# Kernel tuning notes

Hardware: AMD Instinct MI355X
Metric: run time of the kernel (lower is better)

## Reference

```python
import jax, jax.numpy as jnp
import numpy as np

B, N, D = 32, 540, 512
H = 8
DH = D // H
MAX_LEN = 540
POS_CLIP = MAX_LEN - 1


def setup_inputs() -> dict:
    key = jax.random.key(0)
    ks = jax.random.split(key, 12)
    s = 0.02
    inp = {
        "query": jax.random.normal(ks[0], (B, N, D), dtype=jnp.float32),
        "Wq": jax.random.normal(ks[1], (D, D), dtype=jnp.float32) * s,
        "bq": jnp.zeros((D,), jnp.float32),
        "Wk": jax.random.normal(ks[2], (D, D), dtype=jnp.float32) * s,
        "bk": jnp.zeros((D,), jnp.float32),
        "Wv": jax.random.normal(ks[3], (D, D), dtype=jnp.float32) * s,
        "bv": jnp.zeros((D,), jnp.float32),
        "Wh": jax.random.normal(ks[4], (D, D), dtype=jnp.float32) * s,
        "bh": jnp.zeros((D,), jnp.float32),
        "pos_k": jax.random.uniform(ks[5], (2 * POS_CLIP + 1, DH), dtype=jnp.float32, minval=-0.05, maxval=0.05),
        "gamma": jnp.ones((D,), jnp.float32),
        "beta": jnp.zeros((D,), jnp.float32),
        "valid_len": jax.random.randint(ks[6], (B,), 1, N + 1, dtype=jnp.int32),
    }
    return inp


def _split_heads(x):
    # [B, N, D] -> [H*B, N, DH], head-major on axis 0 (matches tf.concat(tf.split(x,H,-1),0))
    return x.reshape(B, N, H, DH).transpose(2, 0, 1, 3).reshape(H * B, N, DH)


def reference(query, Wq, bq, Wk, bk, Wv, bv, Wh, bh, pos_k, gamma, beta, valid_len):
    q = _split_heads(query @ Wq + bq)  # [HB, N, DH]
    k = _split_heads(query @ Wk + bk)
    v = _split_heads(query @ Wv + bv)

    QK = jnp.einsum("xqd,xkd->xqk", q, k)  # [HB, N, N]

    # relative position bias (Shaw et al. 2018)
    rel = jnp.arange(N)[None, :] - jnp.arange(N)[:, None]
    rel = jnp.clip(rel, -POS_CLIP, POS_CLIP) + POS_CLIP
    pos_enc_k = pos_k[rel]  # [N, N, DH]
    QR = jnp.einsum("xqd,qkd->xqk", q, pos_enc_k)

    attn = (QK + QR) / jnp.sqrt(jnp.float32(DH))

    # key-side sequence mask, broadcast over heads and query rows
    key_mask = jnp.arange(N)[None, :] < valid_len[:, None]  # [B, N]
    key_mask = jnp.tile(key_mask[:, None, :], (H, N, 1))  # [HB, N, N]
    attn = jnp.where(key_mask, attn, jnp.float32(-1e12))
    attn = jax.nn.softmax(attn, axis=-1)

    out = jnp.einsum("xqk,xkd->xqd", attn, v)  # [HB, N, DH]
    out = out.reshape(H, B, N, DH).transpose(1, 2, 0, 3).reshape(B, N, D)
    out = out @ Wh + bh
    out = out + query

    # layer norm over last axis
    mean = jnp.mean(out, axis=-1, keepdims=True)
    var = jnp.mean(jnp.square(out - mean), axis=-1, keepdims=True)
    normalized = (out - mean) * jax.lax.rsqrt(var + 1e-7)
    return gamma * normalized + beta
```

## Files before the change

### kernel.cpp

```cpp
#include <hip/hip_runtime.h>
#include <hip/hip_bf16.h>

typedef __hip_bfloat16 bf16;

#define NB 32
#define NSEQ 540
#define ND 512
#define NH 8
#define NDH 64
#define NHB 256
#define NM 17280
#define NPOS 1079
#define VTP 544

typedef __bf16 v8bf __attribute__((ext_vector_type(8)));
typedef float f32x4 __attribute__((ext_vector_type(4)));

union U8 {
  uint4 u;
  unsigned short s[8];
  v8bf v;
};

union U2 {
  uint2 u;
  unsigned short s[4];
};

__device__ __forceinline__ unsigned short f2b(float x) {
  union { float f; unsigned u; } c;
  c.f = x;
  const unsigned r = c.u + 0x7fffu + ((c.u >> 16) & 1u);
  return (unsigned short)(r >> 16);
}

__device__ __forceinline__ float b2f16(unsigned short s) {
  return __uint_as_float(((unsigned)s) << 16);
}

__device__ __forceinline__ void bar_lds() {
  asm volatile("s_waitcnt lgkmcnt(0)\n\ts_barrier" ::: "memory");
}

__device__ __forceinline__ int xcd_swz(int p, int total) {
  const int g = p >> 5, r = p & 31;
  return ((g << 5) + 32 <= total) ? ((g << 5) + ((r & 7) << 2) + (r >> 3)) : p;
}

__device__ __forceinline__ void gl_lds16(const unsigned short* g,
                                         unsigned short* l) {
  __builtin_amdgcn_global_load_lds(
      (const __attribute__((address_space(1))) unsigned int*)g,
      (__attribute__((address_space(3))) unsigned int*)l, 16, 0, 0);
}

__device__ __forceinline__ void cvt16(const float* __restrict__ p,
                                      unsigned short* __restrict__ dst) {
  unsigned short s[16];
#pragma unroll
  for (int i = 0; i < 4; i++) {
    const float4 v = *(const float4*)(p + i * 4);
    s[i * 4 + 0] = f2b(v.x);
    s[i * 4 + 1] = f2b(v.y);
    s[i * 4 + 2] = f2b(v.z);
    s[i * 4 + 3] = f2b(v.w);
  }
  *(uint4*)dst = *(uint4*)s;
  *(uint4*)(dst + 8) = *(uint4*)(s + 8);
}

__global__ __launch_bounds__(256) void prep(const float* __restrict__ x,
                                            unsigned short* __restrict__ xb,
                                            const float* __restrict__ pos,
                                            unsigned short* __restrict__ posb) {
  const int blk = blockIdx.x;
  if (blk < 4320) {
    const int i = blk * 256 + threadIdx.x;
    const float4 a = *(const float4*)(x + (size_t)i * 8);
    const float4 b = *(const float4*)(x + (size_t)i * 8 + 4);
    unsigned short s[8];
    s[0] = f2b(a.x); s[1] = f2b(a.y); s[2] = f2b(a.z); s[3] = f2b(a.w);
    s[4] = f2b(b.x); s[5] = f2b(b.y); s[6] = f2b(b.z); s[7] = f2b(b.w);
    *(uint4*)(xb + (size_t)i * 8) = *(uint4*)s;
  } else {
    const int i = (blk - 4320) * 256 + threadIdx.x;
    if (i < NPOS * NDH) posb[i] = f2b(pos[i]);
  }
}

__global__ __launch_bounds__(256) void wcvt(
    const float* __restrict__ Wq, const float* __restrict__ Wk,
    const float* __restrict__ Wv, const float* __restrict__ Wh,
    unsigned short* __restrict__ Wt) {
  __shared__ unsigned short T[64][72];
  const int tid = threadIdx.x;
  const int sel = blockIdx.z;
  const float* W = (sel == 0) ? Wq : (sel == 1) ? Wk : (sel == 2) ? Wv : Wh;
  unsigned short* out = Wt + (size_t)sel * ND * ND;
  const int k0 = blockIdx.x * 64, n0 = blockIdx.y * 64;
  const int r = tid >> 2, g = tid & 3;
  cvt16(W + (size_t)(k0 + r) * ND + n0 + g * 16, &T[r][g * 16]);
  __syncthreads();
  unsigned short s[16];
#pragma unroll
  for (int j = 0; j < 16; j++) s[j] = T[g * 16 + j][r];
  unsigned short* dst = out + (size_t)(n0 + r) * ND + k0 + g * 16;
  *(uint4*)dst = *(uint4*)s;
  *(uint4*)(dst + 8) = *(uint4*)(s + 8);
}

#define GEMM_CORE_B16(APTR)                                                       \
  {                                                                               \
    const int lrow = lane >> 2;                                                   \
    const int lc8 = (lane & 3) * 8;                                               \
    const int arow = 32 * w + lrow;                   \
    const unsigned short* ga = APTR + (size_t)(m0 + arow) * ND + lc8;             \
    const unsigned short* gb = Bt + (size_t)(n0 + arow) * ND + lc8;               \
    gl_lds16(ga, &As[0][(2 * w) * 512]);                                          \
    gl_lds16(ga + 16 * ND, &As[0][(2 * w) * 512 + 512]);                          \
    gl_lds16(gb, &Bs[0][(2 * w) * 512]);                                          \
    gl_lds16(gb + 16 * ND, &Bs[0][(2 * w) * 512 + 512]);                          \
    __syncthreads();                                                              \
    for (int t = 0; t < 16; t++) {                                                \
      const int cur = t & 1;                                                      \
      if (t < 15) {                                                               \
        const int k1 = (t + 1) * 32;                                              \
        gl_lds16(ga + k1, &As[cur ^ 1][(2 * w) * 512]);                           \
        gl_lds16(ga + k1 + 16 * ND, &As[cur ^ 1][(2 * w) * 512 + 512]);           \
        gl_lds16(gb + k1, &Bs[cur ^ 1][(2 * w) * 512]);                           \
        gl_lds16(gb + k1 + 16 * ND, &Bs[cur ^ 1][(2 * w) * 512 + 512]);           \
      }                                                                           \
      U8 af[4], bfr[4];                                                           \
      _Pragma("unroll")                                                           \
      for (int mi = 0; mi < 4; mi++)                                              \
        af[mi].u = *(const uint4*)&As[cur][(wr * 64 + mi * 16 + l15) * 32 +       \
                                           quad * 8];                             \
      _Pragma("unroll")                                                           \
      for (int ni = 0; ni < 4; ni++)                                              \
        bfr[ni].u = *(const uint4*)&Bs[cur][(wc * 64 + ni * 16 + l15) * 32 +      \
                                            quad * 8];                            \
      _Pragma("unroll")                                                           \
      for (int mi = 0; mi < 4; mi++)                                              \
        _Pragma("unroll")                                                         \
        for (int ni = 0; ni < 4; ni++)                                            \
          acc[mi][ni] = __builtin_amdgcn_mfma_f32_16x16x32_bf16(                  \
              af[mi].v, bfr[ni].v, acc[mi][ni], 0, 0, 0);                         \
      __syncthreads();                                                            \
    }                                                                             \
  }

__global__ __launch_bounds__(256, 3) void qkv_mfma(
    const unsigned short* __restrict__ Xb, const unsigned short* __restrict__ Wt,
    const float* __restrict__ bq, const float* __restrict__ bk,
    const float* __restrict__ bv,
    bf16* __restrict__ qh, bf16* __restrict__ kh, bf16* __restrict__ vt) {
  __shared__ unsigned short As[2][4096];
  __shared__ unsigned short Bs[2][4096];
  const int tid = threadIdx.x;
  const int phys = blockIdx.x + (blockIdx.y << 2) + 540 * blockIdx.z;
  const int W = xcd_swz(phys, 1620);
  const int sel = W / 540;
  const int rem = W - sel * 540;
  const int m0 = (rem >> 2) * 128, n0 = (rem & 3) * 128;
  const unsigned short* Bt = Wt + (size_t)sel * ND * ND;
  const float* bias = (sel == 0) ? bq : (sel == 1) ? bk : bv;
  const int lane = tid & 63, w = tid >> 6;
  const int wr = w & 1, wc = w >> 1;
  const int l15 = lane & 15, quad = lane >> 4;

  f32x4 acc[4][4];
#pragma unroll
  for (int mi = 0; mi < 4; mi++)
#pragma unroll
    for (int ni = 0; ni < 4; ni++) acc[mi][ni] = (f32x4){0.f, 0.f, 0.f, 0.f};

  GEMM_CORE_B16(Xb)

  if (sel != 2) {
    unsigned short* o = (unsigned short*)((sel == 0) ? qh : kh);
#pragma unroll
    for (int mi = 0; mi < 4; mi++) {
      const int m = m0 + wr * 64 + mi * 16 + quad * 4;
      const int bidx = m / NSEQ;
      const int seq0 = m - bidx * NSEQ;
#pragma unroll
      for (int ni = 0; ni < 4; ni++) {
        const int n = n0 + wc * 64 + ni * 16 + l15;
        const int h = n >> 6, dh = n & 63;
        const float bsv = bias[n];
        const size_t base = (((size_t)(h * NB + bidx)) * NSEQ + seq0) * NDH + dh;
#pragma unroll
        for (int i = 0; i < 4; i++)
          o[base + (size_t)i * NDH] = f2b(acc[mi][ni][i] + bsv);
      }
    }
  } else {
    unsigned short* o = (unsigned short*)vt;
#pragma unroll
    for (int mi = 0; mi < 4; mi++) {
      const int m = m0 + wr * 64 + mi * 16 + quad * 4;
      const int bidx = m / NSEQ;
      const int seq0 = m - bidx * NSEQ;
#pragma unroll
      for (int ni = 0; ni < 4; ni++) {
        const int n = n0 + wc * 64 + ni * 16 + l15;
        const int h = n >> 6, dh = n & 63;
        const float bsv = bias[n];
        unsigned short pk[4];
#pragma unroll
        for (int i = 0; i < 4; i++) pk[i] = f2b(acc[mi][ni][i] + bsv);
        *(uint2*)(o + (((size_t)(h * NB + bidx)) * NDH + dh) * VTP + seq0) =
            *(uint2*)pk;
      }
    }
  }
}

__global__ __launch_bounds__(256, 3) void out_mfma(
    const unsigned short* __restrict__ ctxb, const unsigned short* __restrict__ Wht,
    const float* __restrict__ bh, const float* __restrict__ query,
    float* __restrict__ tmp) {
  __shared__ unsigned short As[2][4096];
  __shared__ unsigned short Bs[2][4096];
  const int tid = threadIdx.x;
  const unsigned short* Bt = Wht;
  const int phys = blockIdx.x + (blockIdx.y << 2);
  const int W = xcd_swz(phys, 540);
  const int m0 = (W >> 2) * 128, n0 = (W & 3) * 128;
  const int lane = tid & 63, w = tid >> 6;
  const int wr = w & 1, wc = w >> 1;
  const int l15 = lane & 15, quad = lane >> 4;

  f32x4 acc[4][4];
#pragma unroll
  for (int mi = 0; mi < 4; mi++)
#pragma unroll
    for (int ni = 0; ni < 4; ni++) acc[mi][ni] = (f32x4){0.f, 0.f, 0.f, 0.f};

  GEMM_CORE_B16(ctxb)

#pragma unroll
  for (int mi = 0; mi < 4; mi++) {
    const int m = m0 + wr * 64 + mi * 16 + quad * 4;
#pragma unroll
    for (int ni = 0; ni < 4; ni++) {
      const int n = n0 + wc * 64 + ni * 16 + l15;
      const float bsv = bh[n];
#pragma unroll
      for (int i = 0; i < 4; i++) {
        const size_t off = (size_t)(m + i) * ND + n;
        tmp[off] = acc[mi][ni][i] + bsv + query[off];
      }
    }
  }
}

#define PW 584

__global__ __launch_bounds__(256, 6) void attn(
    const bf16* __restrict__ qh, const bf16* __restrict__ kh,
    const bf16* __restrict__ vt, const unsigned short* __restrict__ posb,
    const int* __restrict__ vlen, bf16* __restrict__ ctx) {
  __shared__ unsigned short P[16][PW];
  __shared__ float Tt[16][84];
  __shared__ float red4[16][4];
  __shared__ float sinv[16];

  const int tid = threadIdx.x;
  const int lane = tid & 63;
  const int w = tid >> 6;
  const int l15 = lane & 15;
  const int quad = lane >> 4;
  const int qb = blockIdx.x;
  const int x = blockIdx.y;
  const int b = x & 31, h = x >> 5;
  const int q0 = qb * 16;
  const int valid = vlen[b];
  const int NT = (valid + 63) >> 6;
  const int NC = (valid + 31) >> 5;
  const bf16* qbase = qh + (size_t)x * NSEQ * NDH;
  const unsigned short* kbase = (const unsigned short*)(kh + (size_t)x * NSEQ * NDH);
  const unsigned short* vbase = (const unsigned short*)(vt + (size_t)x * NDH * VTP);

  U8 aq0, aq1;
  {
    const int q = q0 + l15;
    if (q < NSEQ) {
      aq0.u = *(const uint4*)(qbase + (size_t)q * NDH + quad * 8);
      aq1.u = *(const uint4*)(qbase + (size_t)q * NDH + 32 + quad * 8);
    } else {
      aq0.u = make_uint4(0, 0, 0, 0);
      aq1.u = make_uint4(0, 0, 0, 0);
    }
  }

  U8 ck0, ck1, cp0, cp1, ce0, ce1;
  {
    const int key = w * 16 + l15;
    ck0.u = *(const uint4*)(kbase + (size_t)key * NDH + quad * 8);
    ck1.u = *(const uint4*)(kbase + (size_t)key * NDH + 32 + quad * 8);
    const long pr = (long)(524 - q0 + w * 16 + l15);
    cp0.u = *(const uint4*)(posb + pr * NDH + quad * 8);
    cp1.u = *(const uint4*)(posb + pr * NDH + 32 + quad * 8);
    if (w == 0) {
      const long pr2 = (long)(524 - q0 + 64 + l15);
      ce0.u = *(const uint4*)(posb + pr2 * NDH + quad * 8);
      ce1.u = *(const uint4*)(posb + pr2 * NDH + 32 + quad * 8);
    }
  }

  float pmax1 = -1e30f;

  for (int kt = 0; kt < NT; kt++) {
    U8 nk0, nk1, np0, np1, ne0, ne1;
    if (kt < NT - 1) {
      const int k1 = kt * 64 + 64;
      const int key = k1 + w * 16 + l15;
      nk0.u = *(const uint4*)(kbase + (size_t)key * NDH + quad * 8);
      nk1.u = *(const uint4*)(kbase + (size_t)key * NDH + 32 + quad * 8);
      const long pr = (long)(k1 - q0 + 524 + w * 16 + l15);
      np0.u = *(const uint4*)(posb + pr * NDH + quad * 8);
      np1.u = *(const uint4*)(posb + pr * NDH + 32 + quad * 8);
      if (w == 0) {
        const long pr2 = (long)(k1 - q0 + 524 + 64 + l15);
        ne0.u = *(const uint4*)(posb + pr2 * NDH + quad * 8);
        ne1.u = *(const uint4*)(posb + pr2 * NDH + 32 + quad * 8);
      }
    }

    f32x4 accqk = {0.f, 0.f, 0.f, 0.f};
    accqk = __builtin_amdgcn_mfma_f32_16x16x32_bf16(ck0.v, aq0.v, accqk, 0, 0, 0);
    accqk = __builtin_amdgcn_mfma_f32_16x16x32_bf16(ck1.v, aq1.v, accqk, 0, 0, 0);
    f32x4 accT = {0.f, 0.f, 0.f, 0.f};
    accT = __builtin_amdgcn_mfma_f32_16x16x32_bf16(cp0.v, aq0.v, accT, 0, 0, 0);
    accT = __builtin_amdgcn_mfma_f32_16x16x32_bf16(cp1.v, aq1.v, accT, 0, 0, 0);
    f32x4 accT2 = {0.f, 0.f, 0.f, 0.f};
    if (w == 0) {
      accT2 = __builtin_amdgcn_mfma_f32_16x16x32_bf16(ce0.v, aq0.v, accT2, 0, 0, 0);
      accT2 = __builtin_amdgcn_mfma_f32_16x16x32_bf16(ce1.v, aq1.v, accT2, 0, 0, 0);
    }

    bar_lds();
    *(f32x4*)&Tt[l15][w * 16 + quad * 4] = accT;
    if (w == 0) *(f32x4*)&Tt[l15][64 + quad * 4] = accT2;
    bar_lds();
    {
      const int k0 = kt * 64;
      const int cb = w * 16 + quad * 4;
      const int jb = cb + 15 - l15;
      U2 pk;
      float pm = -1e30f;
#pragma unroll
      for (int i = 0; i < 4; i++) {
        const float v = (accqk[i] + Tt[l15][jb + i]) * 0.125f;
        pk.s[i] = f2b(v);
        const bool cm = (k0 + cb + i) < valid;
        pm = fmaxf(pm, cm ? v : -1e30f);
      }
      *(uint2*)&P[l15][k0 + cb] = pk.u;
      pmax1 = fmaxf(pmax1, pm);
    }
    ck0 = nk0; ck1 = nk1; cp0 = np0; cp1 = np1;
    if (w == 0) { ce0 = ne0; ce1 = ne1; }
  }

  pmax1 = fmaxf(pmax1, __shfl_xor(pmax1, 16, 64));
  pmax1 = fmaxf(pmax1, __shfl_xor(pmax1, 32, 64));
  if (quad == 0) red4[l15][w] = pmax1;

  const int dh = w * 16 + l15;
  const unsigned short* vrow = vbase + (size_t)dh * VTP;
  U8 cv;
  cv.u = *(const uint4*)(vrow + quad * 8);

  bar_lds();

  {
    const int r = tid >> 4, c = tid & 15;
    const float4 rm = *(const float4*)red4[r];
    const float rowmax = fmaxf(fmaxf(rm.x, rm.y), fmaxf(rm.z, rm.w));
    const int nv = (valid + 7) >> 3;
    float sl = 0.f;
    for (int ch = c; ch < nv; ch += 16) {
      const uint4 u = *(const uint4*)&P[r][ch * 8];
      unsigned ue[4];
#pragma unroll
      for (int jj = 0; jj < 4; jj++) {
        const unsigned uu = ((const unsigned*)&u)[jj];
        const float lo = __uint_as_float(uu << 16);
        const float hi = __uint_as_float(uu & 0xffff0000u);
        float el = __expf(lo - rowmax);
        float eh = __expf(hi - rowmax);
        const int cb = ch * 8 + jj * 2;
        el = (cb < valid) ? el : 0.f;
        eh = (cb + 1 < valid) ? eh : 0.f;
        sl += el + eh;
        ue[jj] = (unsigned)f2b(el) | ((unsigned)f2b(eh) << 16);
      }
      *(uint4*)&P[r][ch * 8] = *(const uint4*)ue;
    }
    for (int ch = c; ch < 72; ch += 16) {
      if (ch >= nv) *(uint4*)&P[r][ch * 8] = make_uint4(0, 0, 0, 0);
    }
#pragma unroll
    for (int m = 1; m < 16; m <<= 1) sl += __shfl_xor(sl, m, 16);
    if (c == 0) sinv[r] = 1.f / sl;
  }
  bar_lds();

  f32x4 acco = {0.f, 0.f, 0.f, 0.f};
  for (int ci = 0; ci < NC; ci++) {
    U8 nv_;
    if (ci + 1 < NC) nv_.u = *(const uint4*)(vrow + (ci + 1) * 32 + quad * 8);
    U8 ap;
    ap.u = *(const uint4*)&P[l15][ci * 32 + quad * 8];
    acco = __builtin_amdgcn_mfma_f32_16x16x32_bf16(ap.v, cv.v, acco, 0, 0, 0);
    cv = nv_;
  }
  unsigned short* ob = (unsigned short*)ctx;
#pragma unroll
  for (int i = 0; i < 4; i++) {
    const int q = q0 + quad * 4 + i;
    if (q < NSEQ) {
      ob[((size_t)b * NSEQ + q) * ND + h * NDH + dh] =
          f2b(acco[i] * sinv[quad * 4 + i]);
    }
  }
}

__global__ __launch_bounds__(256) void lnorm(
    const float* __restrict__ tmp, const float* __restrict__ gamma,
    const float* __restrict__ beta, float* __restrict__ out) {
  const int w = threadIdx.x >> 6, lane = threadIdx.x & 63;
  const int row = blockIdx.x * 4 + w;
  const size_t base = (size_t)row * 512 + lane * 8;
  const float4 a = *(const float4*)(tmp + base);
  const float4 b = *(const float4*)(tmp + base + 4);

  float s = a.x + a.y + a.z + a.w + b.x + b.y + b.z + b.w;
#pragma unroll
  for (int m = 1; m < 64; m <<= 1) s += __shfl_xor(s, m, 64);
  const float mean = s * (1.f / 512.f);

  float d[8] = {a.x - mean, a.y - mean, a.z - mean, a.w - mean,
                b.x - mean, b.y - mean, b.z - mean, b.w - mean};
  float v = 0.f;
#pragma unroll
  for (int i = 0; i < 8; i++) v += d[i] * d[i];
#pragma unroll
  for (int m = 1; m < 64; m <<= 1) v += __shfl_xor(v, m, 64);
  const float rstd = rsqrtf(v * (1.f / 512.f) + 1e-7f);

  const int col = lane * 8;
  const float4 g0 = *(const float4*)(gamma + col);
  const float4 g1 = *(const float4*)(gamma + col + 4);
  const float4 be0 = *(const float4*)(beta + col);
  const float4 be1 = *(const float4*)(beta + col + 4);
  float4 o0, o1;
  o0.x = d[0] * rstd * g0.x + be0.x;
  o0.y = d[1] * rstd * g0.y + be0.y;
  o0.z = d[2] * rstd * g0.z + be0.z;
  o0.w = d[3] * rstd * g0.w + be0.w;
  o1.x = d[4] * rstd * g1.x + be1.x;
  o1.y = d[5] * rstd * g1.y + be1.y;
  o1.z = d[6] * rstd * g1.z + be1.z;
  o1.w = d[7] * rstd * g1.w + be1.w;
  *(float4*)(out + base) = o0;
  *(float4*)(out + base + 4) = o1;
}

extern "C" void kernel_launch(void* const* d_in, const int* in_sizes, int n_in,
                              void* d_out, int out_size, void* d_ws, size_t ws_size,
                              hipStream_t stream) {
  const float* query = (const float*)d_in[0];
  const float* Wq = (const float*)d_in[1];
  const float* bq = (const float*)d_in[2];
  const float* Wk = (const float*)d_in[3];
  const float* bk = (const float*)d_in[4];
  const float* Wv = (const float*)d_in[5];
  const float* bv = (const float*)d_in[6];
  const float* Wh = (const float*)d_in[7];
  const float* bh = (const float*)d_in[8];
  const float* pos = (const float*)d_in[9];
  const float* gamma = (const float*)d_in[10];
  const float* beta = (const float*)d_in[11];
  const int* vlen = (const int*)d_in[12];

  bf16* ws = (bf16*)d_ws;
  const size_t QSZ = (size_t)NHB * NSEQ * NDH;
  const size_t VSZ = (size_t)NHB * NDH * VTP;
  bf16* qh = ws;
  bf16* kh = ws + QSZ;
  bf16* vt = ws + 2 * QSZ;
  unsigned short* posb = (unsigned short*)(ws + 2 * QSZ + VSZ);
  unsigned short* Wtb = posb + (size_t)NPOS * NDH;
  unsigned short* Xb = (unsigned short*)d_out;
  bf16* ctx = (bf16*)d_out;
  float* tmp = (float*)d_ws;
  (void)ws_size;

  prep<<<dim3(4590), 256, 0, stream>>>(query, Xb, pos, posb);
  wcvt<<<dim3(8, 8, 4), 256, 0, stream>>>(Wq, Wk, Wv, Wh, Wtb);
  qkv_mfma<<<dim3(4, 135, 3), 256, 0, stream>>>(Xb, Wtb, bq, bk, bv, qh, kh, vt);
  attn<<<dim3(34, 256), 256, 0, stream>>>(qh, kh, vt, posb, vlen, ctx);
  out_mfma<<<dim3(4, 135), 256, 0, stream>>>((const unsigned short*)ctx,
                                             Wtb + 3 * (size_t)ND * ND, bh, query, tmp);
  lnorm<<<dim3(4320), 256, 0, stream>>>(tmp, gamma, beta, (float*)d_out);
}
```

Measured before the change: 309.9 us.

## Merge weight conversion into prep, split QKV GEMM, and vectorize epilogue stores

Folds the weight transpose/convert kernel into the prep kernel, removing one launch. The Q/K projection is split from the V projection. The Q/K and output GEMMs swap the MFMA operands so each lane holds 4 consecutive columns, which allows 8-byte bf16 stores and float4 bias/residual loads instead of scattered scalar stores. The GEMM core also drops LDS double buffering in favour of a single buffer with two barriers per k-step, which halves LDS use but exposes global load latency.

```diff
diff --git a/kernel.cpp b/kernel.cpp
--- a/kernel.cpp
+++ b/kernel.cpp
@@ -69,101 +69,96 @@
   *(uint4*)(dst + 8) = *(uint4*)(s + 8);
 }
 
-__global__ __launch_bounds__(256) void prep(const float* __restrict__ x,
-                                            unsigned short* __restrict__ xb,
-                                            const float* __restrict__ pos,
-                                            unsigned short* __restrict__ posb) {
+__global__ __launch_bounds__(256) void prep(
+    const float* __restrict__ x, unsigned short* __restrict__ xb,
+    const float* __restrict__ pos, unsigned short* __restrict__ posb,
+    const float* __restrict__ Wq, const float* __restrict__ Wk,
+    const float* __restrict__ Wv, const float* __restrict__ Wh,
+    unsigned short* __restrict__ Wt) {
+  __shared__ unsigned short T[64][72];
   const int blk = blockIdx.x;
+  const int tid = threadIdx.x;
   if (blk < 4320) {
-    const int i = blk * 256 + threadIdx.x;
+    const int i = blk * 256 + tid;
     const float4 a = *(const float4*)(x + (size_t)i * 8);
     const float4 b = *(const float4*)(x + (size_t)i * 8 + 4);
     unsigned short s[8];
     s[0] = f2b(a.x); s[1] = f2b(a.y); s[2] = f2b(a.z); s[3] = f2b(a.w);
     s[4] = f2b(b.x); s[5] = f2b(b.y); s[6] = f2b(b.z); s[7] = f2b(b.w);
     *(uint4*)(xb + (size_t)i * 8) = *(uint4*)s;
+  } else if (blk < 4590) {
+    const int i = (blk - 4320) * 256 + tid;
+    if (i < NPOS * NDH) posb[i] = f2b(pos[i]);
   } else {
-    const int i = (blk - 4320) * 256 + threadIdx.x;
-    if (i < NPOS * NDH) posb[i] = f2b(pos[i]);
-  }
-}
-
-__global__ __launch_bounds__(256) void wcvt(
-    const float* __restrict__ Wq, const float* __restrict__ Wk,
-    const float* __restrict__ Wv, const float* __restrict__ Wh,
-    unsigned short* __restrict__ Wt) {
-  __shared__ unsigned short T[64][72];
-  const int tid = threadIdx.x;
-  const int sel = blockIdx.z;
-  const float* W = (sel == 0) ? Wq : (sel == 1) ? Wk : (sel == 2) ? Wv : Wh;
-  unsigned short* out = Wt + (size_t)sel * ND * ND;
-  const int k0 = blockIdx.x * 64, n0 = blockIdx.y * 64;
-  const int r = tid >> 2, g = tid & 3;
-  cvt16(W + (size_t)(k0 + r) * ND + n0 + g * 16, &T[r][g * 16]);
-  __syncthreads();
-  unsigned short s[16];
-#pragma unroll
-  for (int j = 0; j < 16; j++) s[j] = T[g * 16 + j][r];
-  unsigned short* dst = out + (size_t)(n0 + r) * ND + k0 + g * 16;
-  *(uint4*)dst = *(uint4*)s;
-  *(uint4*)(dst + 8) = *(uint4*)(s + 8);
-}
-
-#define GEMM_CORE_B16(APTR)                                                       \
+    const int idx = blk - 4590;
+    const int sel = idx >> 6;
+    const int rem = idx & 63;
+    const float* W = (sel == 0) ? Wq : (sel == 1) ? Wk : (sel == 2) ? Wv : Wh;
+    unsigned short* out = Wt + (size_t)sel * ND * ND;
+    const int k0 = (rem & 7) * 64, n0 = (rem >> 3) * 64;
+    const int r = tid >> 2, g = tid & 3;
+    cvt16(W + (size_t)(k0 + r) * ND + n0 + g * 16, &T[r][g * 16]);
+    __syncthreads();
+    unsigned short s[16];
+#pragma unroll
+    for (int j = 0; j < 16; j++) s[j] = T[g * 16 + j][r];
+    unsigned short* dst = out + (size_t)(n0 + r) * ND + k0 + g * 16;
+    *(uint4*)dst = *(uint4*)s;
+    *(uint4*)(dst + 8) = *(uint4*)(s + 8);
+  }
+}
+
+#define GEMM_STAGE_COMPUTE(APTR, MFMA_LINE)                                       \
   {                                                                               \
     const int lrow = lane >> 2;                                                   \
     const int lc8 = (lane & 3) * 8;                                               \
     const int arow = 32 * w + lrow;                   \
-    const unsigned short* ga = APTR + (size_t)(m0 + arow) * ND + lc8;             \
-    const unsigned short* gb = Bt + (size_t)(n0 + arow) * ND + lc8;               \
-    gl_lds16(ga, &As[0][(2 * w) * 512]);                                          \
-    gl_lds16(ga + 16 * ND, &As[0][(2 * w) * 512 + 512]);                          \
-    gl_lds16(gb, &Bs[0][(2 * w) * 512]);                                          \
-    gl_lds16(gb + 16 * ND, &Bs[0][(2 * w) * 512 + 512]);                          \
-    __syncthreads();                                                              \
-    for (int t = 0; t < 16; t++) {                                                \
-      const int cur = t & 1;                                                      \
-      if (t < 15) {                                                               \
-        const int k1 = (t + 1) * 32;                                              \
-        gl_lds16(ga + k1, &As[cur ^ 1][(2 * w) * 512]);                           \
-        gl_lds16(ga + k1 + 16 * ND, &As[cur ^ 1][(2 * w) * 512 + 512]);           \
-        gl_lds16(gb + k1, &Bs[cur ^ 1][(2 * w) * 512]);                           \
-        gl_lds16(gb + k1 + 16 * ND, &Bs[cur ^ 1][(2 * w) * 512 + 512]);           \
-      }                                                                           \
+    unsigned short* lA0 = &As[0][0] + (size_t)(2 * w) * 512;                      \
+    unsigned short* lB0 = &Bs[0][0] + (size_t)(2 * w) * 512;                      \
+    for (int k0 = 0; k0 < 512; k0 += 32) {                                        \
+      __syncthreads();                                                            \
+      gl_lds16(APTR + (size_t)(m0 + arow) * ND + k0 + lc8, lA0);                  \
+      gl_lds16(APTR + (size_t)(m0 + arow + 16) * ND + k0 + lc8, lA0 + 512);       \
+      gl_lds16(Bt + (size_t)(n0 + arow) * ND + k0 + lc8, lB0);                    \
+      gl_lds16(Bt + (size_t)(n0 + arow + 16) * ND + k0 + lc8, lB0 + 512);         \
+      __syncthreads();                                                            \
       U8 af[4], bfr[4];                                                           \
       _Pragma("unroll")                                                           \
       for (int mi = 0; mi < 4; mi++)                                              \
-        af[mi].u = *(const uint4*)&As[cur][(wr * 64 + mi * 16 + l15) * 32 +       \
-                                           quad * 8];                             \
+        af[mi].u = *(const uint4*)&As[wr * 64 + mi * 16 + l15][quad * 8];         \
       _Pragma("unroll")                                                           \
       for (int ni = 0; ni < 4; ni++)                                              \
-        bfr[ni].u = *(const uint4*)&Bs[cur][(wc * 64 + ni * 16 + l15) * 32 +      \
-                                            quad * 8];                            \
+        bfr[ni].u = *(const uint4*)&Bs[wc * 64 + ni * 16 + l15][quad * 8];        \
       _Pragma("unroll")                                                           \
       for (int mi = 0; mi < 4; mi++)                                              \
         _Pragma("unroll")                                                         \
         for (int ni = 0; ni < 4; ni++)                                            \
-          acc[mi][ni] = __builtin_amdgcn_mfma_f32_16x16x32_bf16(                  \
-              af[mi].v, bfr[ni].v, acc[mi][ni], 0, 0, 0);                         \
-      __syncthreads();                                                            \
+          MFMA_LINE;                                                              \
     }                                                                             \
   }
 
-__global__ __launch_bounds__(256, 3) void qkv_mfma(
+#define GEMM_CORE_B16(APTR)                                                       \
+  GEMM_STAGE_COMPUTE(APTR, acc[mi][ni] = __builtin_amdgcn_mfma_f32_16x16x32_bf16( \
+                               af[mi].v, bfr[ni].v, acc[mi][ni], 0, 0, 0))
+
+#define GEMM_CORE_B16S(APTR)                                                      \
+  GEMM_STAGE_COMPUTE(APTR, acc[mi][ni] = __builtin_amdgcn_mfma_f32_16x16x32_bf16( \
+                               bfr[ni].v, af[mi].v, acc[mi][ni], 0, 0, 0))
+
+__global__ __launch_bounds__(256, 3) void qkv_qk(
     const unsigned short* __restrict__ Xb, const unsigned short* __restrict__ Wt,
     const float* __restrict__ bq, const float* __restrict__ bk,
-    const float* __restrict__ bv,
-    bf16* __restrict__ qh, bf16* __restrict__ kh, bf16* __restrict__ vt) {
-  __shared__ unsigned short As[2][4096];
-  __shared__ unsigned short Bs[2][4096];
+    bf16* __restrict__ qh, bf16* __restrict__ kh) {
+  __shared__ unsigned short As[128][32];
+  __shared__ unsigned short Bs[128][32];
   const int tid = threadIdx.x;
   const int phys = blockIdx.x + (blockIdx.y << 2) + 540 * blockIdx.z;
-  const int W = xcd_swz(phys, 1620);
+  const int W = xcd_swz(phys, 1080);
   const int sel = W / 540;
   const int rem = W - sel * 540;
   const int m0 = (rem >> 2) * 128, n0 = (rem & 3) * 128;
   const unsigned short* Bt = Wt + (size_t)sel * ND * ND;
-  const float* bias = (sel == 0) ? bq : (sel == 1) ? bk : bv;
+  const float* bias = sel ? bk : bq;
   const int lane = tid & 63, w = tid >> 6;
   const int wr = w & 1, wc = w >> 1;
   const int l15 = lane & 15, quad = lane >> 4;
@@ -174,44 +169,67 @@
 #pragma unroll
     for (int ni = 0; ni < 4; ni++) acc[mi][ni] = (f32x4){0.f, 0.f, 0.f, 0.f};
 
+  GEMM_CORE_B16S(Xb)
+
+  unsigned short* o = (unsigned short*)(sel ? kh : qh);
+#pragma unroll
+  for (int mi = 0; mi < 4; mi++) {
+    const int m = m0 + wr * 64 + mi * 16 + l15;
+    const int bidx = m / NSEQ;
+    const int seq0 = m - bidx * NSEQ;
+#pragma unroll
+    for (int ni = 0; ni < 4; ni++) {
+      const int nb = n0 + wc * 64 + ni * 16 + quad * 4;
+      const int h = nb >> 6, dh = nb & 63;
+      const float4 b4 = *(const float4*)(bias + nb);
+      U2 pk;
+      pk.s[0] = f2b(acc[mi][ni][0] + b4.x);
+      pk.s[1] = f2b(acc[mi][ni][1] + b4.y);
+      pk.s[2] = f2b(acc[mi][ni][2] + b4.z);
+      pk.s[3] = f2b(acc[mi][ni][3] + b4.w);
+      *(uint2*)(o + (((size_t)(h * NB + bidx)) * NSEQ + seq0) * NDH + dh) = pk.u;
+    }
+  }
+}
+
+__global__ __launch_bounds__(256, 3) void qkv_v(
+    const unsigned short* __restrict__ Xb, const unsigned short* __restrict__ Wt,
+    const float* __restrict__ bv, bf16* __restrict__ vt) {
+  __shared__ unsigned short As[128][32];
+  __shared__ unsigned short Bs[128][32];
+  const int tid = threadIdx.x;
+  const int phys = blockIdx.x + (blockIdx.y << 2);
+  const int W = xcd_swz(phys, 540);
+  const int m0 = (W >> 2) * 128, n0 = (W & 3) * 128;
+  const unsigned short* Bt = Wt + (size_t)2 * ND * ND;
+  const int lane = tid & 63, w = tid >> 6;
+  const int wr = w & 1, wc = w >> 1;
+  const int l15 = lane & 15, quad = lane >> 4;
+
+  f32x4 acc[4][4];
+#pragma unroll
+  for (int mi = 0; mi < 4; mi++)
+#pragma unroll
+    for (int ni = 0; ni < 4; ni++) acc[mi][ni] = (f32x4){0.f, 0.f, 0.f, 0.f};
+
   GEMM_CORE_B16(Xb)
 
-  if (sel != 2) {
-    unsigned short* o = (unsigned short*)((sel == 0) ? qh : kh);
-#pragma unroll
-    for (int mi = 0; mi < 4; mi++) {
-      const int m = m0 + wr * 64 + mi * 16 + quad * 4;
-      const int bidx = m / NSEQ;
-      const int seq0 = m - bidx * NSEQ;
-#pragma unroll
-      for (int ni = 0; ni < 4; ni++) {
-        const int n = n0 + wc * 64 + ni * 16 + l15;
-        const int h = n >> 6, dh = n & 63;
-        const float bsv = bias[n];
-        const size_t base = (((size_t)(h * NB + bidx)) * NSEQ + seq0) * NDH + dh;
-#pragma unroll
-        for (int i = 0; i < 4; i++)
-          o[base + (size_t)i * NDH] = f2b(acc[mi][ni][i] + bsv);
-      }
-    }
-  } else {
-    unsigned short* o = (unsigned short*)vt;
-#pragma unroll
-    for (int mi = 0; mi < 4; mi++) {
-      const int m = m0 + wr * 64 + mi * 16 + quad * 4;
-      const int bidx = m / NSEQ;
-      const int seq0 = m - bidx * NSEQ;
-#pragma unroll
-      for (int ni = 0; ni < 4; ni++) {
-        const int n = n0 + wc * 64 + ni * 16 + l15;
-        const int h = n >> 6, dh = n & 63;
-        const float bsv = bias[n];
-        unsigned short pk[4];
-#pragma unroll
-        for (int i = 0; i < 4; i++) pk[i] = f2b(acc[mi][ni][i] + bsv);
-        *(uint2*)(o + (((size_t)(h * NB + bidx)) * NDH + dh) * VTP + seq0) =
-            *(uint2*)pk;
-      }
+  unsigned short* o = (unsigned short*)vt;
+#pragma unroll
+  for (int mi = 0; mi < 4; mi++) {
+    const int m = m0 + wr * 64 + mi * 16 + quad * 4;
+    const int bidx = m / NSEQ;
+    const int seq0 = m - bidx * NSEQ;
+#pragma unroll
+    for (int ni = 0; ni < 4; ni++) {
+      const int n = n0 + wc * 64 + ni * 16 + l15;
+      const int h = n >> 6, dh = n & 63;
+      const float bsv = bv[n];
+      unsigned short pk[4];
+#pragma unroll
+      for (int i = 0; i < 4; i++) pk[i] = f2b(acc[mi][ni][i] + bsv);
+      *(uint2*)(o + (((size_t)(h * NB + bidx)) * NDH + dh) * VTP + seq0) =
+          *(uint2*)pk;
     }
   }
 }
@@ -220,8 +238,8 @@
     const unsigned short* __restrict__ ctxb, const unsigned short* __restrict__ Wht,
     const float* __restrict__ bh, const float* __restrict__ query,
     float* __restrict__ tmp) {
-  __shared__ unsigned short As[2][4096];
-  __shared__ unsigned short Bs[2][4096];
+  __shared__ unsigned short As[128][32];
+  __shared__ unsigned short Bs[128][32];
   const int tid = threadIdx.x;
   const unsigned short* Bt = Wht;
   const int phys = blockIdx.x + (blockIdx.y << 2);
@@ -237,20 +255,23 @@
 #pragma unroll
     for (int ni = 0; ni < 4; ni++) acc[mi][ni] = (f32x4){0.f, 0.f, 0.f, 0.f};
 
-  GEMM_CORE_B16(ctxb)
+  GEMM_CORE_B16S(ctxb)
 
 #pragma unroll
   for (int mi = 0; mi < 4; mi++) {
-    const int m = m0 + wr * 64 + mi * 16 + quad * 4;
+    const int m = m0 + wr * 64 + mi * 16 + l15;
 #pragma unroll
     for (int ni = 0; ni < 4; ni++) {
-      const int n = n0 + wc * 64 + ni * 16 + l15;
-      const float bsv = bh[n];
-#pragma unroll
-      for (int i = 0; i < 4; i++) {
-        const size_t off = (size_t)(m + i) * ND + n;
-        tmp[off] = acc[mi][ni][i] + bsv + query[off];
-      }
+      const int nb = n0 + wc * 64 + ni * 16 + quad * 4;
+      const float4 b4 = *(const float4*)(bh + nb);
+      const size_t off = (size_t)m * ND + nb;
+      const float4 q4 = *(const float4*)(query + off);
+      float4 o4;
+      o4.x = acc[mi][ni][0] + b4.x + q4.x;
+      o4.y = acc[mi][ni][1] + b4.y + q4.y;
+      o4.z = acc[mi][ni][2] + b4.z + q4.z;
+      o4.w = acc[mi][ni][3] + b4.w + q4.w;
+      *(float4*)(tmp + off) = o4;
     }
   }
 }
@@ -499,9 +520,9 @@
   float* tmp = (float*)d_ws;
   (void)ws_size;
 
-  prep<<<dim3(4590), 256, 0, stream>>>(query, Xb, pos, posb);
-  wcvt<<<dim3(8, 8, 4), 256, 0, stream>>>(Wq, Wk, Wv, Wh, Wtb);
-  qkv_mfma<<<dim3(4, 135, 3), 256, 0, stream>>>(Xb, Wtb, bq, bk, bv, qh, kh, vt);
+  prep<<<dim3(4846), 256, 0, stream>>>(query, Xb, pos, posb, Wq, Wk, Wv, Wh, Wtb);
+  qkv_qk<<<dim3(4, 135, 2), 256, 0, stream>>>(Xb, Wtb, bq, bk, qh, kh);
+  qkv_v<<<dim3(4, 135), 256, 0, stream>>>(Xb, Wtb, bv, vt);
   attn<<<dim3(34, 256), 256, 0, stream>>>(qh, kh, vt, posb, vlen, ctx);
   out_mfma<<<dim3(4, 135), 256, 0, stream>>>((const unsigned short*)ctx,
                                              Wtb + 3 * (size_t)ND * ND, bh, query, tmp);
```

New measurement: 317.0 us. +2.3%, slower.

## Merge weight conversion into prep kernel and single-buffer GEMM LDS tiles

Applied to the files above, without the earlier changes.

Folds the weight transpose/convert kernel into the prep kernel as extra blocks, which saves one launch. The GEMM core drops its double-buffered LDS prefetch and uses a single buffer with two barriers per k-step, halving shared memory per block. This may allow more resident blocks, but global loads are no longer overlapped with MFMA compute inside a block.

```diff
diff --git a/kernel.cpp b/kernel.cpp
--- a/kernel.cpp
+++ b/kernel.cpp
@@ -69,44 +69,43 @@
   *(uint4*)(dst + 8) = *(uint4*)(s + 8);
 }
 
-__global__ __launch_bounds__(256) void prep(const float* __restrict__ x,
-                                            unsigned short* __restrict__ xb,
-                                            const float* __restrict__ pos,
-                                            unsigned short* __restrict__ posb) {
+__global__ __launch_bounds__(256) void prep(
+    const float* __restrict__ x, unsigned short* __restrict__ xb,
+    const float* __restrict__ pos, unsigned short* __restrict__ posb,
+    const float* __restrict__ Wq, const float* __restrict__ Wk,
+    const float* __restrict__ Wv, const float* __restrict__ Wh,
+    unsigned short* __restrict__ Wt) {
+  __shared__ unsigned short T[64][72];
   const int blk = blockIdx.x;
+  const int tid = threadIdx.x;
   if (blk < 4320) {
-    const int i = blk * 256 + threadIdx.x;
+    const int i = blk * 256 + tid;
     const float4 a = *(const float4*)(x + (size_t)i * 8);
     const float4 b = *(const float4*)(x + (size_t)i * 8 + 4);
     unsigned short s[8];
     s[0] = f2b(a.x); s[1] = f2b(a.y); s[2] = f2b(a.z); s[3] = f2b(a.w);
     s[4] = f2b(b.x); s[5] = f2b(b.y); s[6] = f2b(b.z); s[7] = f2b(b.w);
     *(uint4*)(xb + (size_t)i * 8) = *(uint4*)s;
+  } else if (blk < 4590) {
+    const int i = (blk - 4320) * 256 + tid;
+    if (i < NPOS * NDH) posb[i] = f2b(pos[i]);
   } else {
-    const int i = (blk - 4320) * 256 + threadIdx.x;
-    if (i < NPOS * NDH) posb[i] = f2b(pos[i]);
-  }
-}
-
-__global__ __launch_bounds__(256) void wcvt(
-    const float* __restrict__ Wq, const float* __restrict__ Wk,
-    const float* __restrict__ Wv, const float* __restrict__ Wh,
-    unsigned short* __restrict__ Wt) {
-  __shared__ unsigned short T[64][72];
-  const int tid = threadIdx.x;
-  const int sel = blockIdx.z;
-  const float* W = (sel == 0) ? Wq : (sel == 1) ? Wk : (sel == 2) ? Wv : Wh;
-  unsigned short* out = Wt + (size_t)sel * ND * ND;
-  const int k0 = blockIdx.x * 64, n0 = blockIdx.y * 64;
-  const int r = tid >> 2, g = tid & 3;
-  cvt16(W + (size_t)(k0 + r) * ND + n0 + g * 16, &T[r][g * 16]);
-  __syncthreads();
-  unsigned short s[16];
-#pragma unroll
-  for (int j = 0; j < 16; j++) s[j] = T[g * 16 + j][r];
-  unsigned short* dst = out + (size_t)(n0 + r) * ND + k0 + g * 16;
-  *(uint4*)dst = *(uint4*)s;
-  *(uint4*)(dst + 8) = *(uint4*)(s + 8);
+    const int idx = blk - 4590;
+    const int sel = idx >> 6;
+    const int rem = idx & 63;
+    const float* W = (sel == 0) ? Wq : (sel == 1) ? Wk : (sel == 2) ? Wv : Wh;
+    unsigned short* out = Wt + (size_t)sel * ND * ND;
+    const int k0 = (rem & 7) * 64, n0 = (rem >> 3) * 64;
+    const int r = tid >> 2, g = tid & 3;
+    cvt16(W + (size_t)(k0 + r) * ND + n0 + g * 16, &T[r][g * 16]);
+    __syncthreads();
+    unsigned short s[16];
+#pragma unroll
+    for (int j = 0; j < 16; j++) s[j] = T[g * 16 + j][r];
+    unsigned short* dst = out + (size_t)(n0 + r) * ND + k0 + g * 16;
+    *(uint4*)dst = *(uint4*)s;
+    *(uint4*)(dst + 8) = *(uint4*)(s + 8);
+  }
 }
 
 #define GEMM_CORE_B16(APTR)                                                       \
@@ -114,38 +113,28 @@
     const int lrow = lane >> 2;                                                   \
     const int lc8 = (lane & 3) * 8;                                               \
     const int arow = 32 * w + lrow;                   \
-    const unsigned short* ga = APTR + (size_t)(m0 + arow) * ND + lc8;             \
-    const unsigned short* gb = Bt + (size_t)(n0 + arow) * ND + lc8;               \
-    gl_lds16(ga, &As[0][(2 * w) * 512]);                                          \
-    gl_lds16(ga + 16 * ND, &As[0][(2 * w) * 512 + 512]);                          \
-    gl_lds16(gb, &Bs[0][(2 * w) * 512]);                                          \
-    gl_lds16(gb + 16 * ND, &Bs[0][(2 * w) * 512 + 512]);                          \
-    __syncthreads();                                                              \
-    for (int t = 0; t < 16; t++) {                                                \
-      const int cur = t & 1;                                                      \
-      if (t < 15) {                                                               \
-        const int k1 = (t + 1) * 32;                                              \
-        gl_lds16(ga + k1, &As[cur ^ 1][(2 * w) * 512]);                           \
-        gl_lds16(ga + k1 + 16 * ND, &As[cur ^ 1][(2 * w) * 512 + 512]);           \
-        gl_lds16(gb + k1, &Bs[cur ^ 1][(2 * w) * 512]);                           \
-        gl_lds16(gb + k1 + 16 * ND, &Bs[cur ^ 1][(2 * w) * 512 + 512]);           \
-      }                                                                           \
+    unsigned short* lA0 = &As[0][0] + (size_t)(2 * w) * 512;                      \
+    unsigned short* lB0 = &Bs[0][0] + (size_t)(2 * w) * 512;                      \
+    for (int k0 = 0; k0 < 512; k0 += 32) {                                        \
+      __syncthreads();                                                            \
+      gl_lds16(APTR + (size_t)(m0 + arow) * ND + k0 + lc8, lA0);                  \
+      gl_lds16(APTR + (size_t)(m0 + arow + 16) * ND + k0 + lc8, lA0 + 512);       \
+      gl_lds16(Bt + (size_t)(n0 + arow) * ND + k0 + lc8, lB0);                    \
+      gl_lds16(Bt + (size_t)(n0 + arow + 16) * ND + k0 + lc8, lB0 + 512);         \
+      __syncthreads();                                                            \
       U8 af[4], bfr[4];                                                           \
       _Pragma("unroll")                                                           \
       for (int mi = 0; mi < 4; mi++)                                              \
-        af[mi].u = *(const uint4*)&As[cur][(wr * 64 + mi * 16 + l15) * 32 +       \
-                                           quad * 8];                             \
+        af[mi].u = *(const uint4*)&As[wr * 64 + mi * 16 + l15][quad * 8];         \
       _Pragma("unroll")                                                           \
       for (int ni = 0; ni < 4; ni++)                                              \
-        bfr[ni].u = *(const uint4*)&Bs[cur][(wc * 64 + ni * 16 + l15) * 32 +      \
-                                            quad * 8];                            \
+        bfr[ni].u = *(const uint4*)&Bs[wc * 64 + ni * 16 + l15][quad * 8];        \
       _Pragma("unroll")                                                           \
       for (int mi = 0; mi < 4; mi++)                                              \
         _Pragma("unroll")                                                         \
         for (int ni = 0; ni < 4; ni++)                                            \
           acc[mi][ni] = __builtin_amdgcn_mfma_f32_16x16x32_bf16(                  \
               af[mi].v, bfr[ni].v, acc[mi][ni], 0, 0, 0);                         \
-      __syncthreads();                                                            \
     }                                                                             \
   }
 
@@ -154,8 +143,8 @@
     const float* __restrict__ bq, const float* __restrict__ bk,
     const float* __restrict__ bv,
     bf16* __restrict__ qh, bf16* __restrict__ kh, bf16* __restrict__ vt) {
-  __shared__ unsigned short As[2][4096];
-  __shared__ unsigned short Bs[2][4096];
+  __shared__ unsigned short As[128][32];
+  __shared__ unsigned short Bs[128][32];
   const int tid = threadIdx.x;
   const int phys = blockIdx.x + (blockIdx.y << 2) + 540 * blockIdx.z;
   const int W = xcd_swz(phys, 1620);
@@ -220,8 +209,8 @@
     const unsigned short* __restrict__ ctxb, const unsigned short* __restrict__ Wht,
     const float* __restrict__ bh, const float* __restrict__ query,
     float* __restrict__ tmp) {
-  __shared__ unsigned short As[2][4096];
-  __shared__ unsigned short Bs[2][4096];
+  __shared__ unsigned short As[128][32];
+  __shared__ unsigned short Bs[128][32];
   const int tid = threadIdx.x;
   const unsigned short* Bt = Wht;
   const int phys = blockIdx.x + (blockIdx.y << 2);
@@ -499,8 +488,7 @@
   float* tmp = (float*)d_ws;
   (void)ws_size;
 
-  prep<<<dim3(4590), 256, 0, stream>>>(query, Xb, pos, posb);
-  wcvt<<<dim3(8, 8, 4), 256, 0, stream>>>(Wq, Wk, Wv, Wh, Wtb);
+  prep<<<dim3(4846), 256, 0, stream>>>(query, Xb, pos, posb, Wq, Wk, Wv, Wh, Wtb);
   qkv_mfma<<<dim3(4, 135, 3), 256, 0, stream>>>(Xb, Wtb, bq, bk, bv, qh, kh, vt);
   attn<<<dim3(34, 256), 256, 0, stream>>>(qh, kh, vt, posb, vlen, ctx);
   out_mfma<<<dim3(4, 135), 256, 0, stream>>>((const unsigned short*)ctx,
```

Result: no change. 304.7 us (-1.7%).
